# Optimization experiments

Hardware: AMD Instinct MI355X
Metric: run time of the kernel (lower is better)

## Reference

```python
import jax, jax.numpy as jnp
import numpy as np

K_NEIGHBORS = 10
SINKHORN_REG = 0.1
SINKHORN_ITERS = 50
EPS = 1e-10


def _pairwise_dist(x):
    # Euclidean cdist; clamp avoids sqrt(0) NaN grads on the diagonal
    sq = jnp.sum(x * x, axis=1)
    d2 = sq[:, None] + sq[None, :] - 2.0 * (x @ x.T)
    return jnp.sqrt(jnp.maximum(d2, 1e-12))


def setup_inputs() -> dict:
    key = jax.random.key(0)
    k1, k2 = jax.random.split(key)
    n, d = 8192, 128
    return {
        "embeddings": jax.random.normal(k1, (n, d), dtype=jnp.float32),
        "reference_embeddings": jax.random.normal(k2, (n, d), dtype=jnp.float32),
    }


def reference(embeddings, reference_embeddings):
    k = min(K_NEIGHBORS, embeddings.shape[0] - 1)

    cur_d = _pairwise_dist(embeddings)              # [n, n]
    ref_d = _pairwise_dist(reference_embeddings)    # [n, n]

    # k+1 smallest (ascending), drop self-distance column
    cur_knn = jnp.sort(cur_d, axis=1)[:, 1:k + 1]   # [n, k]
    ref_knn = jnp.sort(ref_d, axis=1)[:, 1:k + 1]   # [n, k]

    a = cur_knn / (jnp.sum(cur_knn, axis=1, keepdims=True) + EPS)  # [n, k]
    b = ref_knn / (jnp.sum(ref_knn, axis=1, keepdims=True) + EPS)  # [n, k]

    idx = jnp.arange(k, dtype=jnp.float32)
    M = jnp.abs(idx[None, :] - idx[:, None]) / k    # [k, k] shared cost
    Kmat = jnp.exp(-M / SINKHORN_REG)               # [k, k]

    # Batched Sinkhorn across all n samples at once
    def step(u, _):
        v = b / (u @ Kmat + EPS)          # K.T @ u per sample (K symmetric; explicit form u @ K)
        u = a / (v @ Kmat.T + EPS)        # K @ v per sample
        return u, None

    u0 = jnp.ones_like(a)
    u, _ = jax.lax.scan(step, u0, None, length=SINKHORN_ITERS)
    v = b / (u @ Kmat + EPS)

    # sum_ij u_i K_ij M_ij v_j per sample, then mean over n
    per_sample = jnp.einsum('ni,ij,nj->n', u, Kmat * M, v)
    return jnp.mean(per_sample)
```

## Files before the change

kernel.cpp:

```cpp
#include <hip/hip_runtime.h>
#include <hip/hip_bf16.h>
#include <math.h>

#define N 8192
#define D 128
#define NELEM (N * D)
#define KNN 10
#define EPSF 1e-10f
#define CB 256
#define RT 64
#define NSLICE 8
#define RH 1024

typedef unsigned short ushort_t;
typedef short bf16x8 __attribute__((ext_vector_type(8)));
typedef float f32x4 __attribute__((ext_vector_type(4)));

template <int L>
__device__ __forceinline__ void insM(float (&l)[L], float v) {
  #pragma unroll
  for (int q = L - 1; q >= 1; --q)
    l[q] = __builtin_amdgcn_fmed3f(l[q - 1], l[q], v);
  l[0] = fminf(l[0], v);
}

__global__ void prep_kernel(const float* __restrict__ xc,
                            const float* __restrict__ xr,
                            ushort_t* __restrict__ xb,
                            ushort_t* __restrict__ xa,
                            float* __restrict__ sq) {
  int wid  = (blockIdx.x * blockDim.x + threadIdx.x) >> 6;
  int lane = threadIdx.x & 63;
  if (wid >= 2 * N) return;
  const float* x = (wid < N) ? xc : xr;
  int row = (wid < N) ? wid : wid - N;
  float2 v = *reinterpret_cast<const float2*>(x + (size_t)row * D + lane * 2);
  float s = v.x * v.x + v.y * v.y;
  #pragma unroll
  for (int off = 32; off; off >>= 1) s += __shfl_xor(s, off, 64);
  if (lane == 0) sq[wid] = s;
  auto cvt = [](float f) -> unsigned int {
    unsigned int b = __float_as_uint(f);
    return (b + 0x7FFFu + ((b >> 16) & 1u)) >> 16;
  };
  unsigned int pb = cvt(v.x) | (cvt(v.y) << 16);
  unsigned int pa = cvt(-2.f * v.x) | (cvt(-2.f * v.y) << 16);
  *reinterpret_cast<unsigned int*>(xb + (size_t)wid * D + lane * 2) = pb;
  *reinterpret_cast<unsigned int*>(xa + (size_t)wid * D + lane * 2) = pa;
}

__global__ __launch_bounds__(256) void knn_mfma(
    const ushort_t* __restrict__ xb,
    const ushort_t* __restrict__ xa,
    const float* __restrict__ sq,
    float* __restrict__ partial) {
  __shared__ __align__(16) ushort_t Albuf[2][RT * D];
  __shared__ float sqbuf[2][RT];

  const int bid = blockIdx.x;
  const int mat = bid >> 8;
  const int colblk = (bid >> 3) & 31;
  const int slice = bid & 7;
  const ushort_t* __restrict__ XB = xb + (size_t)mat * NELEM;
  const ushort_t* __restrict__ XA = xa + (size_t)mat * NELEM;
  const float* __restrict__ SQ = sq + mat * N;
  const int r0 = slice * RH;
  const int t = threadIdx.x;
  const int w = t >> 6, l = t & 63;
  const int c0 = colblk * CB + w * 64;

  bf16x8 bfr[4][4];
  #pragma unroll
  for (int j = 0; j < 4; ++j) {
    const ushort_t* p = XB + (size_t)(c0 + j * 16 + (l & 15)) * D + (l >> 4) * 8;
    #pragma unroll
    for (int kk = 0; kk < 4; ++kk)
      bfr[j][kk] = *reinterpret_cast<const bf16x8*>(p + kk * 32);
  }

  float cand[4][11];
  #pragma unroll
  for (int j = 0; j < 4; ++j)
    #pragma unroll
    for (int q = 0; q < 11; ++q) cand[j][q] = 3.4e38f;

  auto stage = [&](int tt, int bb) {
    const ushort_t* rowg = XA + (size_t)(r0 + tt * RT) * D;
    #pragma unroll
    for (int k2 = 0; k2 < 4; ++k2) {
      int s = w * 256 + k2 * 64 + l;
      int row = s >> 4, chslot = s & 15;
      int ch = (chslot & 8) | ((chslot & 7) ^ (row & 7));
      const ushort_t* g = rowg + row * D + ch * 8;
      ushort_t* dst = &Albuf[bb][(w * 256 + k2 * 64) * 8];
      __builtin_amdgcn_global_load_lds(
          (const __attribute__((address_space(1))) void*)g,
          (__attribute__((address_space(3))) void*)dst, 16, 0, 0);
    }
    if (w == 0) {
      const float* gs = SQ + r0 + tt * RT + l;
      float* dsts = &sqbuf[bb][0];
      __builtin_amdgcn_global_load_lds(
          (const __attribute__((address_space(1))) void*)gs,
          (__attribute__((address_space(3))) void*)dsts, 4, 0, 0);
    }
  };

  stage(0, 0);
  asm volatile("s_waitcnt vmcnt(0)" ::: "memory");
  __syncthreads();

  for (int tt = 0; tt < RH / RT; ++tt) {
    const int cur = tt & 1;
    if (tt < RH / RT - 1) stage(tt + 1, cur ^ 1);

    f32x4 sqi[4];
    #pragma unroll
    for (int i = 0; i < 4; ++i)
      sqi[i] = *reinterpret_cast<const f32x4*>(&sqbuf[cur][i * 16 + (l >> 4) * 4]);

    f32x4 acc[4][4];
    #pragma unroll
    for (int i = 0; i < 4; ++i)
      #pragma unroll
      for (int j = 0; j < 4; ++j) acc[i][j] = sqi[i];

    #pragma unroll
    for (int kk = 0; kk < 4; ++kk) {
      const int ch = kk * 4 + (l >> 4);
      const int chs = (ch & 8) | ((ch & 7) ^ (l & 7));
      bf16x8 af[4];
      #pragma unroll
      for (int i = 0; i < 4; ++i) {
        const int row = i * 16 + (l & 15);
        af[i] = *reinterpret_cast<const bf16x8*>(&Albuf[cur][(row * 16 + chs) * 8]);
      }
      #pragma unroll
      for (int i = 0; i < 4; ++i)
        #pragma unroll
        for (int j = 0; j < 4; ++j)
          acc[i][j] = __builtin_amdgcn_mfma_f32_16x16x32_bf16(af[i], bfr[j][kk],
                                                              acc[i][j], 0, 0, 0);
    }

    #pragma unroll
    for (int r = 0; r < 4; ++r)
      #pragma unroll
      for (int i = 0; i < 4; ++i)
        #pragma unroll
        for (int j = 0; j < 4; ++j)
          insM<11>(cand[j], acc[i][j][r]);

    asm volatile("s_waitcnt vmcnt(0)" ::: "memory");
    __syncthreads();
  }

  #pragma unroll
  for (int step = 16; step <= 32; step <<= 1)
    #pragma unroll
    for (int j = 0; j < 4; ++j)
      #pragma unroll
      for (int q = 0; q < 11; ++q) {
        float o = __shfl_xor(cand[j][q], step, 64);
        insM<11>(cand[j], o);
      }

  if (l < 16) {
    #pragma unroll
    for (int j = 0; j < 4; ++j) {
      const int c = c0 + j * 16 + l;
      const int selfin = (c >= r0 && c < r0 + RH) ? 1 : 0;
      float* dst = partial + ((size_t)(mat * N + c) * NSLICE + slice) * KNN;
      #pragma unroll
      for (int q = 0; q < KNN; ++q) dst[q] = cand[j][q + selfin];
    }
  }
}

__global__ void merge_kernel(const float* __restrict__ partial,
                             const float* __restrict__ sq,
                             float* __restrict__ knn) {
  int idx = blockIdx.x * blockDim.x + threadIdx.x;
  if (idx >= 2 * N) return;
  float best[KNN];
  #pragma unroll
  for (int q = 0; q < KNN; ++q) best[q] = 3.4e38f;
  const float* p = partial + (size_t)idx * NSLICE * KNN;
  for (int s = 0; s < NSLICE * KNN; ++s) insM<KNN>(best, p[s]);
  const float sqc = sq[idx];
  #pragma unroll
  for (int q = 0; q < KNN; ++q) {
    float d2 = best[q] + sqc;
    knn[(size_t)idx * KNN + q] = sqrtf(fmaxf(d2, 1e-12f));
  }
}

__global__ void sinkhorn_kernel(const float* __restrict__ knnc,
                                const float* __restrict__ knnr,
                                float* __restrict__ ps) {
  int s = blockIdx.x * blockDim.x + threadIdx.x;
  if (s >= N) return;
  constexpr float E1 = 0.36787944117144233f;
  float a[KNN], b[KNN];
  float suma = 0.f, sumb = 0.f;
  #pragma unroll
  for (int q = 0; q < KNN; ++q) { a[q] = knnc[(size_t)s * KNN + q]; suma += a[q]; }
  #pragma unroll
  for (int q = 0; q < KNN; ++q) { b[q] = knnr[(size_t)s * KNN + q]; sumb += b[q]; }
  float rsa = __builtin_amdgcn_rcpf(suma + EPSF);
  float rsb = __builtin_amdgcn_rcpf(sumb + EPSF);
  #pragma unroll
  for (int q = 0; q < KNN; ++q) { a[q] *= rsa; b[q] *= rsb; }

  float u_[KNN], v_[KNN];
  #pragma unroll
  for (int q = 0; q < KNN; ++q) u_[q] = 1.f;

  #pragma unroll 1
  for (int it = 0; it < 50; ++it) {
    float L[KNN], S[KNN];
    L[0] = u_[0];
    #pragma unroll
    for (int q = 1; q < KNN; ++q) L[q] = fmaf(E1, L[q - 1], u_[q]);
    S[KNN - 1] = u_[KNN - 1];
    #pragma unroll
    for (int q = KNN - 2; q >= 0; --q) S[q] = fmaf(E1, S[q + 1], u_[q]);
    #pragma unroll
    for (int q = 0; q < KNN; ++q) {
      float den = (q < KNN - 1) ? fmaf(E1, S[q + 1], L[q]) : L[KNN - 1];
      v_[q] = b[q] * __builtin_amdgcn_rcpf(den + EPSF);
    }
    L[0] = v_[0];
    #pragma unroll
    for (int q = 1; q < KNN; ++q) L[q] = fmaf(E1, L[q - 1], v_[q]);
    S[KNN - 1] = v_[KNN - 1];
    #pragma unroll
    for (int q = KNN - 2; q >= 0; --q) S[q] = fmaf(E1, S[q + 1], v_[q]);
    #pragma unroll
    for (int q = 0; q < KNN; ++q) {
      float den = (q < KNN - 1) ? fmaf(E1, S[q + 1], L[q]) : L[KNN - 1];
      u_[q] = a[q] * __builtin_amdgcn_rcpf(den + EPSF);
    }
  }
  {
    float L[KNN], S[KNN];
    L[0] = u_[0];
    #pragma unroll
    for (int q = 1; q < KNN; ++q) L[q] = fmaf(E1, L[q - 1], u_[q]);
    S[KNN - 1] = u_[KNN - 1];
    #pragma unroll
    for (int q = KNN - 2; q >= 0; --q) S[q] = fmaf(E1, S[q + 1], u_[q]);
    #pragma unroll
    for (int q = 0; q < KNN; ++q) {
      float den = (q < KNN - 1) ? fmaf(E1, S[q + 1], L[q]) : L[KNN - 1];
      v_[q] = b[q] * __builtin_amdgcn_rcpf(den + EPSF);
    }
  }
  float cost = 0.f;
  #pragma unroll
  for (int i = 0; i < KNN; ++i) {
    float accr = 0.f;
    #pragma unroll
    for (int j = 0; j < KNN; ++j) {
      const int dd = i > j ? i - j : j - i;
      const float w = 0.1f * (float)dd * __builtin_expf(-(float)dd);
      accr = fmaf(w, v_[j], accr);
    }
    cost = fmaf(u_[i], accr, cost);
  }
  ps[s] = cost;
}

__global__ void reduce_kernel(const float* __restrict__ ps, float* __restrict__ out) {
  __shared__ float red[256];
  int tid = threadIdx.x;
  float s = 0.f;
  for (int i = tid; i < N; i += 256) s += ps[i];
  red[tid] = s;
  __syncthreads();
  #pragma unroll
  for (int off = 128; off > 0; off >>= 1) {
    if (tid < off) red[tid] += red[tid + off];
    __syncthreads();
  }
  if (tid == 0) out[0] = red[0] * (1.0f / N);
}

extern "C" void kernel_launch(void* const* d_in, const int* in_sizes, int n_in,
                              void* d_out, int out_size, void* d_ws, size_t ws_size,
                              hipStream_t stream) {
  const float* xc = (const float*)d_in[0];
  const float* xr = (const float*)d_in[1];
  float* out = (float*)d_out;
  char* wsb = (char*)d_ws;

  float* sq       = (float*)wsb;
  ushort_t* xb    = (ushort_t*)(wsb + (1u << 16));
  ushort_t* xa    = (ushort_t*)(wsb + (1u << 16) + (4u << 20));
  float* partial  = (float*)(wsb + (1u << 16) + (8u << 20));
  float* knn      = partial + (size_t)2 * N * NSLICE * KNN;
  float* ps       = knn + (size_t)2 * N * KNN;

  prep_kernel<<<dim3(2 * N / 4), dim3(256), 0, stream>>>(xc, xr, xb, xa, sq);
  knn_mfma<<<dim3(512), dim3(256), 0, stream>>>(xb, xa, sq, partial);
  merge_kernel<<<dim3((2 * N + 255) / 256), dim3(256), 0, stream>>>(partial, sq, knn);
  sinkhorn_kernel<<<dim3(N / 64), dim3(64), 0, stream>>>(knn, knn + (size_t)N * KNN, ps);
  reduce_kernel<<<dim3(1), dim3(256), 0, stream>>>(ps, out);
}
```

Before: 134.6 us.

## Halve per-wave column tile, double grid, and mask self-distance explicitly

Each wave now covers 32 columns instead of 64, and the grid grows from 512 to 1024 blocks, with launch bounds set to 4 blocks per CU. This spreads work across more CUs and cuts register pressure: fewer accumulators, and candidate lists of 10 instead of 11. The self-distance entry is now overwritten with a large value only in the tile that contains the diagonal, so the extra candidate slot is no longer needed. In exchange, each A tile loaded into LDS feeds half as many MFMAs, so LDS and global traffic per unit of compute doubles.

Measured after the change: 110.6 us. 17.8% less time.

```diff
diff --git a/kernel.cpp b/kernel.cpp
--- a/kernel.cpp
+++ b/kernel.cpp
@@ -7,10 +7,10 @@
 #define NELEM (N * D)
 #define KNN 10
 #define EPSF 1e-10f
-#define CB 256
 #define RT 64
 #define NSLICE 8
 #define RH 1024
+#define BIGF 3.0e38f
 
 typedef unsigned short ushort_t;
 typedef short bf16x8 __attribute__((ext_vector_type(8)));
@@ -49,7 +49,7 @@
   *reinterpret_cast<unsigned int*>(xa + (size_t)wid * D + lane * 2) = pa;
 }
 
-__global__ __launch_bounds__(256) void knn_mfma(
+__global__ __launch_bounds__(256, 4) void knn_mfma(
     const ushort_t* __restrict__ xb,
     const ushort_t* __restrict__ xa,
     const float* __restrict__ sq,
@@ -58,8 +58,8 @@
   __shared__ float sqbuf[2][RT];
 
   const int bid = blockIdx.x;
-  const int mat = bid >> 8;
-  const int colblk = (bid >> 3) & 31;
+  const int mat = bid >> 9;
+  const int colblk = (bid >> 3) & 63;
   const int slice = bid & 7;
   const ushort_t* __restrict__ XB = xb + (size_t)mat * NELEM;
   const ushort_t* __restrict__ XA = xa + (size_t)mat * NELEM;
@@ -67,22 +67,22 @@
   const int r0 = slice * RH;
   const int t = threadIdx.x;
   const int w = t >> 6, l = t & 63;
-  const int c0 = colblk * CB + w * 64;
-
-  bf16x8 bfr[4][4];
-  #pragma unroll
-  for (int j = 0; j < 4; ++j) {
-    const ushort_t* p = XB + (size_t)(c0 + j * 16 + (l & 15)) * D + (l >> 4) * 8;
+  const int c0w = colblk * 128 + w * 32;
+
+  bf16x8 bfr[2][4];
+  #pragma unroll
+  for (int j = 0; j < 2; ++j) {
+    const ushort_t* p = XB + (size_t)(c0w + j * 16 + (l & 15)) * D + (l >> 4) * 8;
     #pragma unroll
     for (int kk = 0; kk < 4; ++kk)
       bfr[j][kk] = *reinterpret_cast<const bf16x8*>(p + kk * 32);
   }
 
-  float cand[4][11];
-  #pragma unroll
-  for (int j = 0; j < 4; ++j)
-    #pragma unroll
-    for (int q = 0; q < 11; ++q) cand[j][q] = 3.4e38f;
+  float cand[2][KNN];
+  #pragma unroll
+  for (int j = 0; j < 2; ++j)
+    #pragma unroll
+    for (int q = 0; q < KNN; ++q) cand[j][q] = BIGF;
 
   auto stage = [&](int tt, int bb) {
     const ushort_t* rowg = XA + (size_t)(r0 + tt * RT) * D;
@@ -119,11 +119,11 @@
     for (int i = 0; i < 4; ++i)
       sqi[i] = *reinterpret_cast<const f32x4*>(&sqbuf[cur][i * 16 + (l >> 4) * 4]);
 
-    f32x4 acc[4][4];
+    f32x4 acc[4][2];
     #pragma unroll
     for (int i = 0; i < 4; ++i)
       #pragma unroll
-      for (int j = 0; j < 4; ++j) acc[i][j] = sqi[i];
+      for (int j = 0; j < 2; ++j) acc[i][j] = sqi[i];
 
     #pragma unroll
     for (int kk = 0; kk < 4; ++kk) {
@@ -138,18 +138,32 @@
       #pragma unroll
       for (int i = 0; i < 4; ++i)
         #pragma unroll
-        for (int j = 0; j < 4; ++j)
+        for (int j = 0; j < 2; ++j)
           acc[i][j] = __builtin_amdgcn_mfma_f32_16x16x32_bf16(af[i], bfr[j][kk],
                                                               acc[i][j], 0, 0, 0);
     }
 
-    #pragma unroll
-    for (int r = 0; r < 4; ++r)
+    const int rbase = r0 + tt * RT;
+    const unsigned diff = (unsigned)(c0w - rbase);
+    if (diff < 64u) {
       #pragma unroll
       for (int i = 0; i < 4; ++i)
         #pragma unroll
-        for (int j = 0; j < 4; ++j)
-          insM<11>(cand[j], acc[i][j][r]);
+        for (int j = 0; j < 2; ++j) {
+          const int rr = (int)diff + j * 16 + (l & 15) - i * 16 - ((l >> 4) << 2);
+          #pragma unroll
+          for (int r = 0; r < 4; ++r)
+            if (rr == r) acc[i][j][r] = BIGF;
+        }
+    }
+
+    #pragma unroll
+    for (int r = 0; r < 4; ++r)
+      #pragma unroll
+      for (int i = 0; i < 4; ++i)
+        #pragma unroll
+        for (int j = 0; j < 2; ++j)
+          insM<KNN>(cand[j], acc[i][j][r]);
 
     asm volatile("s_waitcnt vmcnt(0)" ::: "memory");
     __syncthreads();
@@ -158,21 +172,20 @@
   #pragma unroll
   for (int step = 16; step <= 32; step <<= 1)
     #pragma unroll
-    for (int j = 0; j < 4; ++j)
-      #pragma unroll
-      for (int q = 0; q < 11; ++q) {
+    for (int j = 0; j < 2; ++j)
+      #pragma unroll
+      for (int q = 0; q < KNN; ++q) {
         float o = __shfl_xor(cand[j][q], step, 64);
-        insM<11>(cand[j], o);
+        insM<KNN>(cand[j], o);
       }
 
   if (l < 16) {
     #pragma unroll
-    for (int j = 0; j < 4; ++j) {
-      const int c = c0 + j * 16 + l;
-      const int selfin = (c >= r0 && c < r0 + RH) ? 1 : 0;
+    for (int j = 0; j < 2; ++j) {
+      const int c = c0w + j * 16 + l;
       float* dst = partial + ((size_t)(mat * N + c) * NSLICE + slice) * KNN;
       #pragma unroll
-      for (int q = 0; q < KNN; ++q) dst[q] = cand[j][q + selfin];
+      for (int q = 0; q < KNN; ++q) dst[q] = cand[j][q];
     }
   }
 }
@@ -184,7 +197,7 @@
   if (idx >= 2 * N) return;
   float best[KNN];
   #pragma unroll
-  for (int q = 0; q < KNN; ++q) best[q] = 3.4e38f;
+  for (int q = 0; q < KNN; ++q) best[q] = BIGF;
   const float* p = partial + (size_t)idx * NSLICE * KNN;
   for (int s = 0; s < NSLICE * KNN; ++s) insM<KNN>(best, p[s]);
   const float sqc = sq[idx];
@@ -263,8 +276,8 @@
     #pragma unroll
     for (int j = 0; j < KNN; ++j) {
       const int dd = i > j ? i - j : j - i;
-      const float w = 0.1f * (float)dd * __builtin_expf(-(float)dd);
-      accr = fmaf(w, v_[j], accr);
+      const float wgt = 0.1f * (float)dd * __builtin_expf(-(float)dd);
+      accr = fmaf(wgt, v_[j], accr);
     }
     cost = fmaf(u_[i], accr, cost);
   }
@@ -302,7 +315,7 @@
   float* ps       = knn + (size_t)2 * N * KNN;
 
   prep_kernel<<<dim3(2 * N / 4), dim3(256), 0, stream>>>(xc, xr, xb, xa, sq);
-  knn_mfma<<<dim3(512), dim3(256), 0, stream>>>(xb, xa, sq, partial);
+  knn_mfma<<<dim3(1024), dim3(256), 0, stream>>>(xb, xa, sq, partial);
   merge_kernel<<<dim3((2 * N + 255) / 256), dim3(256), 0, stream>>>(partial, sq, knn);
   sinkhorn_kernel<<<dim3(N / 64), dim3(64), 0, stream>>>(knn, knn + (size_t)N * KNN, ps);
   reduce_kernel<<<dim3(1), dim3(256), 0, stream>>>(ps, out);
```
